# Performance work log

Measured on AMD Instinct MI355X. Metric: run time of the kernel, lower is better.

Reference implementation:

```python
import jax, jax.numpy as jnp
import numpy as np

NUM_HEADS = 8
WINDOW = 7
DILATION = 1
EPS = 1e-5


def channel_ln(x, w, b):
    # x: [B, C, H, W]; normalize over channel dim (axis=1)
    mu = jnp.mean(x, axis=1, keepdims=True)
    var = jnp.var(x, axis=1, keepdims=True)
    xhat = (x - mu) * jax.lax.rsqrt(var + EPS)
    return xhat * w[None, :, None, None] + b[None, :, None, None]


def local_mask(H, W, window, dilation):
    r = (window // 2) * dilation
    ii, jj = jnp.meshgrid(jnp.arange(H), jnp.arange(W), indexing="ij")
    ii = ii.reshape(-1)
    jj = jj.reshape(-1)
    di = jnp.abs(ii[:, None] - ii[None, :])
    dj = jnp.abs(jj[:, None] - jj[None, :])
    m = (di <= r) & (dj <= r)
    if dilation > 1:
        m = m & (di % dilation == 0) & (dj % dilation == 0)
    return m  # [N, N] bool


def local_attention(x, qkv_w, qkv_b, proj_w, proj_b):
    B, C, H, W = x.shape
    N = H * W
    hd = C // NUM_HEADS
    t = x.reshape(B, C, N).transpose(0, 2, 1)            # [B, N, C]
    qkv = t @ qkv_w.T + qkv_b                            # [B, N, 3C]
    qkv = qkv.reshape(B, N, 3, NUM_HEADS, hd)
    q, k, v = (qkv[:, :, i].transpose(0, 2, 1, 3) for i in range(3))  # [B,h,N,d]
    scale = 1.0 / jnp.sqrt(jnp.asarray(hd, x.dtype))
    scores = jnp.einsum("bhnd,bhmd->bhnm", q, k) * scale  # [B,h,N,N]
    mask = local_mask(H, W, WINDOW, DILATION)             # [N,N]
    scores = jnp.where(mask[None, None], scores, jnp.asarray(-jnp.inf, x.dtype))
    attn = jax.nn.softmax(scores, axis=-1)
    out = jnp.einsum("bhnm,bhmd->bhnd", attn, v)          # [B,h,N,d]
    out = out.transpose(0, 2, 1, 3).reshape(B, N, C)      # [B,N,C]
    out = out @ proj_w.T + proj_b
    return out.transpose(0, 2, 1).reshape(B, C, H, W)


def mlp2d(x, fc1_w, fc1_b, fc2_w, fc2_b):
    # 1x1 convs == per-pixel linear over channels
    h = jnp.einsum("bchw,oc->bohw", x, fc1_w) + fc1_b[None, :, None, None]
    h = jax.nn.gelu(h, approximate=False)
    return jnp.einsum("bchw,oc->bohw", h, fc2_w) + fc2_b[None, :, None, None]


def setup_inputs() -> dict:
    key = jax.random.key(0)
    ks = jax.random.split(key, 12)
    B, C, H, W = 1, 256, 56, 56
    hidden = 4 * C
    s = lambda fan: 1.0 / np.sqrt(fan)
    return {
        "x": jax.random.normal(ks[0], (B, C, H, W), jnp.float32),
        "norm1_w": jnp.ones((C,), jnp.float32),
        "norm1_b": jnp.zeros((C,), jnp.float32),
        "qkv_w": jax.random.normal(ks[1], (3 * C, C), jnp.float32) * s(C),
        "qkv_b": jnp.zeros((3 * C,), jnp.float32),
        "proj_w": jax.random.normal(ks[2], (C, C), jnp.float32) * s(C),
        "proj_b": jnp.zeros((C,), jnp.float32),
        "norm2_w": jnp.ones((C,), jnp.float32),
        "norm2_b": jnp.zeros((C,), jnp.float32),
        "fc1_w": jax.random.normal(ks[3], (hidden, C), jnp.float32) * s(C),
        "fc1_b": jnp.zeros((hidden,), jnp.float32),
        "fc2_w": jax.random.normal(ks[4], (C, hidden), jnp.float32) * s(hidden),
        "fc2_b": jnp.zeros((C,), jnp.float32),
    }


def reference(x, norm1_w, norm1_b, qkv_w, qkv_b, proj_w, proj_b,
              norm2_w, norm2_b, fc1_w, fc1_b, fc2_w, fc2_b):
    x = x + local_attention(channel_ln(x, norm1_w, norm1_b), qkv_w, qkv_b, proj_w, proj_b)
    x = x + mlp2d(channel_ln(x, norm2_w, norm2_b), fc1_w, fc1_b, fc2_w, fc2_b)
    return x
```

## Files before the change

### kernel.cpp

```cpp
#include <hip/hip_runtime.h>
#include <math.h>


typedef unsigned int uint;
typedef unsigned short ushort;
typedef unsigned long long u64;
typedef __attribute__((ext_vector_type(8))) short short8;
typedef __attribute__((ext_vector_type(4))) float floatx4;
typedef __attribute__((ext_vector_type(4))) unsigned short ushort4v;

#define AS1(p) (const __attribute__((address_space(1))) void*)(p)
#define AS3(p) (__attribute__((address_space(3))) void*)(p)

__device__ __forceinline__ float bf2f(ushort u) {
  union { uint i; float f; } v; v.i = ((uint)u) << 16; return v.f;
}
__device__ __forceinline__ ushort f2bf(float f) {
  union { float f; uint i; } v; v.f = f;
  uint u = v.i;
  return (ushort)((u + 0x7fffu + ((u >> 16) & 1u)) >> 16);
}

__device__ __forceinline__ void stage64(const ushort* src, int kstride,
                                        ushort* dstBase, int tid) {
  const int srow = tid >> 5;
  const int scb  = (tid & 31) ^ srow;
  const ushort* g = src + (size_t)srow * kstride + scb * 8;
  ushort* d = dstBase + tid * 8;
  #pragma unroll
  for (int r = 0; r < 8; ++r) {
    __builtin_amdgcn_global_load_lds(AS1(g), AS3(d), 16, 0, 0);
    g += 8 * kstride;
    d += 2048;
  }
}

__device__ __forceinline__ void compute64(const ushort* As, const ushort* Bs,
                                          int w, int lane, floatx4 acc[4]) {
  const int fm = lane & 15;
  const int q  = lane >> 4;
  const int swz = fm & 7;
  const int arow = (w * 16 + fm) * 256;
  #pragma unroll
  for (int kt = 0; kt < 8; ++kt) {
    const int blk = ((kt * 4 + q) ^ swz) * 8;
    short8 af = *(const short8*)&As[arow + blk];
    #pragma unroll
    for (int nt = 0; nt < 4; ++nt) {
      short8 bfr = *(const short8*)&Bs[(nt * 16 + fm) * 256 + blk];
      acc[nt] = __builtin_amdgcn_mfma_f32_16x16x32_bf16(af, bfr, acc[nt], 0, 0, 0);
    }
  }
}

__global__ __launch_bounds__(256) void prep_kernel(
    const float* __restrict__ x, const float* __restrict__ n1w,
    const float* __restrict__ n1b,
    const float* __restrict__ qkvw, const float* __restrict__ projw,
    const float* __restrict__ f1w, const float* __restrict__ f2w,
    float* __restrict__ xT, ushort* __restrict__ t1, ushort* __restrict__ wcat)
{
  const int tid = threadIdx.x;
  const int bid = blockIdx.x;
  if (bid >= 196) {
    int idx = (bid - 196) * 256 + tid;
    float v;
    if (idx < 196608)       v = qkvw[idx];
    else if (idx < 262144)  v = projw[idx - 196608];
    else if (idx < 524288)  v = f1w[idx - 262144];
    else                    v = f2w[idx - 524288];
    wcat[idx] = f2bf(v);
    return;
  }
  __shared__ float tile[256 * 17];
  __shared__ float red[2][16][16];
  __shared__ float mu[16], rsv[16];
  const int n0 = bid * 16;
  const int px = tid & 15, grp = tid >> 4;
  #pragma unroll 4
  for (int it = 0; it < 16; ++it) {
    int c = it * 16 + grp;
    tile[c * 17 + px] = x[(size_t)c * 3136 + n0 + px];
  }
  __syncthreads();
  float s = 0.f, ss = 0.f;
  #pragma unroll
  for (int i = 0; i < 16; ++i) {
    float v = tile[(grp * 16 + i) * 17 + px];
    s += v; ss += v * v;
  }
  red[0][px][grp] = s; red[1][px][grp] = ss;
  __syncthreads();
  if (tid < 16) {
    float s2 = 0.f, ss2 = 0.f;
    #pragma unroll
    for (int g = 0; g < 16; ++g) { s2 += red[0][tid][g]; ss2 += red[1][tid][g]; }
    float m = s2 * (1.f / 256.f);
    float var = ss2 * (1.f / 256.f) - m * m;
    mu[tid] = m;
    rsv[tid] = rsqrtf(var + 1e-5f);
  }
  __syncthreads();
  const float wc = n1w[tid], bc = n1b[tid];
  #pragma unroll 4
  for (int p = 0; p < 16; ++p) {
    float v = tile[tid * 17 + p];
    xT[(size_t)(n0 + p) * 256 + tid] = v;
    t1[(size_t)(n0 + p) * 256 + tid] = f2bf((v - mu[p]) * rsv[p] * wc + bc);
  }
}

__global__ __launch_bounds__(256, 2) void qkv_kernel(
    const ushort* __restrict__ A, const ushort* __restrict__ B,
    const float* __restrict__ bias, ushort* __restrict__ out)
{
  __shared__ ushort As[16384], Bs[16384];
  const int tid = threadIdx.x, lane = tid & 63, w = tid >> 6;
  const int m0 = blockIdx.y * 64, n0 = blockIdx.x * 64;
  floatx4 acc[4] = {{0.f,0.f,0.f,0.f},{0.f,0.f,0.f,0.f},
                    {0.f,0.f,0.f,0.f},{0.f,0.f,0.f,0.f}};
  stage64(A + (size_t)m0 * 256, 256, As, tid);
  stage64(B + (size_t)n0 * 256, 256, Bs, tid);
  asm volatile("s_waitcnt vmcnt(0)" ::: "memory");
  __syncthreads();
  compute64(As, Bs, w, lane, acc);
  const int fm = lane & 15, q4 = (lane >> 4) * 4;
  #pragma unroll
  for (int nt = 0; nt < 4; ++nt)
    #pragma unroll
    for (int r = 0; r < 4; ++r) {
      int m = m0 + w * 16 + q4 + r;
      int n = n0 + nt * 16 + fm;
      float v = acc[nt][r] + bias[n];
      if (n < 256) v *= 0.17677669529663687f;
      out[(size_t)m * 768 + n] = f2bf(v);
    }
}

#define ATTN_SMEM 144416

__global__ __launch_bounds__(256, 1) void attnproj_kernel(
    const ushort* __restrict__ qkv, const ushort* __restrict__ pw_bf,
    const float* __restrict__ projb, const float* __restrict__ xT,
    float* __restrict__ x1)
{
  __shared__ __align__(16) char smem[ATTN_SMEM];
  ushort* Kh  = (ushort*)smem;
  ushort* Vh  = (ushort*)(smem + 52000);
  float*  pr  = (float*)(smem + 103200);
  ushort* aas = (ushort*)(smem + 135968);
  ushort* Bs0 = (ushort*)smem;
  ushort* Bs1 = (ushort*)(smem + 103200);

  const int tid = threadIdx.x;
  const int i0 = (blockIdx.x / 14) * 4, j0 = (blockIdx.x % 14) * 4;

  for (int s = tid; s < 3200; s += 256) {
    int p = s >> 5, ck = s & 31;
    int ii = i0 - 3 + p / 10, jj = j0 - 3 + p % 10;
    if (ii >= 0 && ii < 56 && jj >= 0 && jj < 56) {
      const ushort* kr = qkv + (size_t)(ii * 56 + jj) * 768 + 256 + ck * 8;
      short8 kv = *(const short8*)kr;
      u64 lo = ((const u64*)&kv)[0], hi = ((const u64*)&kv)[1];
      *(u64*)&Kh[p * 260 + ck * 8] = lo;
      *(u64*)&Kh[p * 260 + ck * 8 + 4] = hi;
      *(short8*)&Vh[p * 256 + ck * 8] = *(const short8*)(kr + 256);
    } else {
      *(u64*)&Kh[p * 260 + ck * 8] = 0ull;
      *(u64*)&Kh[p * 260 + ck * 8 + 4] = 0ull;
      short8 z = {0, 0, 0, 0, 0, 0, 0, 0};
      *(short8*)&Vh[p * 256 + ck * 8] = z;
    }
  }
  __syncthreads();

  const int wv = tid >> 6, lane = tid & 63;
  const int h = lane >> 3, mg = lane & 7;
  for (int qq = 0; qq < 4; ++qq) {
    const int p = wv * 4 + qq;
    const int qi = p >> 2, qj = p & 3;
    const int iq = i0 + qi, jq = j0 + qj;
    const ushort* qp = qkv + (size_t)(iq * 56 + jq) * 768 + h * 32;
    float qf[32];
    #pragma unroll
    for (int u = 0; u < 4; ++u) {
      short8 qv = *(const short8*)(qp + u * 8);
      #pragma unroll
      for (int e = 0; e < 8; ++e) qf[u * 8 + e] = bf2f((ushort)qv[e]);
    }
    float sv[7];
    float mx = -1e30f;
    #pragma unroll
    for (int k = 0; k < 7; ++k) {
      int m = mg + 8 * k;
      float s = -1e30f;
      if (m < 49) {
        int mi = m / 7, mj = m % 7;
        int ii = iq + mi - 3, jj = jq + mj - 3;
        if (ii >= 0 && ii < 56 && jj >= 0 && jj < 56) {
          int hrow = (qi + mi) * 10 + (qj + mj);
          const u64* k8 = (const u64*)&Kh[hrow * 260 + h * 32];
          float a = 0.f;
          #pragma unroll
          for (int u = 0; u < 8; ++u) {
            u64 kv = k8[u];
            #pragma unroll
            for (int e = 0; e < 4; ++e)
              a += qf[u * 4 + e] * bf2f((ushort)(kv >> (16 * e)));
          }
          s = a;
        }
      }
      sv[k] = s;
      mx = fmaxf(mx, s);
    }
    mx = fmaxf(mx, __shfl_xor(mx, 1));
    mx = fmaxf(mx, __shfl_xor(mx, 2));
    mx = fmaxf(mx, __shfl_xor(mx, 4));
    float sm = 0.f;
    #pragma unroll
    for (int k = 0; k < 7; ++k) { sv[k] = __expf(sv[k] - mx); sm += sv[k]; }
    sm += __shfl_xor(sm, 1);
    sm += __shfl_xor(sm, 2);
    sm += __shfl_xor(sm, 4);
    float inv = 1.f / sm;
    #pragma unroll
    for (int k = 0; k < 7; ++k) {
      int m = mg + 8 * k;
      pr[(p * 8 + h) * 64 + m] = sv[k] * inv;
    }
  }
  __syncthreads();

  stage64(pw_bf, 256, Bs0, tid);

  {
    const int qsel = tid >> 5, cg = tid & 31, hh = cg >> 2;
    #pragma unroll
    for (int pass = 0; pass < 2; ++pass) {
      const int p = pass * 8 + qsel;
      const int qi = p >> 2, qj = p & 3;
      float acc8[8] = {0, 0, 0, 0, 0, 0, 0, 0};
      #pragma unroll
      for (int mi = 0; mi < 7; ++mi)
        #pragma unroll
        for (int mj = 0; mj < 7; ++mj) {
          int m = mi * 7 + mj;
          int hrow = (qi + mi) * 10 + (qj + mj);
          float pm = pr[(p * 8 + hh) * 64 + m];
          short8 v8 = *(const short8*)&Vh[hrow * 256 + cg * 8];
          #pragma unroll
          for (int e = 0; e < 8; ++e)
            acc8[e] += pm * bf2f((ushort)v8[e]);
        }
      short8 o;
      #pragma unroll
      for (int e = 0; e < 8; ++e) o[e] = (short)f2bf(acc8[e]);
      *(short8*)&aas[p * 264 + cg * 8] = o;
    }
  }
  __syncthreads();

  const int fm = lane & 15, q = lane >> 4, q4 = q * 4;
  for (int c = 0; c < 4; ++c) {
    if (c > 0) __syncthreads();
    if (c < 3) {
      stage64(pw_bf + (size_t)(c + 1) * 64 * 256, 256, (c & 1) ? Bs0 : Bs1, tid);
      asm volatile("s_waitcnt vmcnt(8)" ::: "memory");
    } else {
      asm volatile("s_waitcnt vmcnt(0)" ::: "memory");
    }
    __syncthreads();
    const ushort* Bc = (c & 1) ? Bs1 : Bs0;
    floatx4 acc = {0.f, 0.f, 0.f, 0.f};
    const int rr = wv * 16 + fm;
    #pragma unroll
    for (int kt = 0; kt < 8; ++kt) {
      short8 af = *(const short8*)&aas[fm * 264 + kt * 32 + q * 8];
      short8 bfr = *(const short8*)&Bc[rr * 256 + (((kt * 4 + q) ^ (fm & 7))) * 8];
      acc = __builtin_amdgcn_mfma_f32_16x16x32_bf16(af, bfr, acc, 0, 0, 0);
    }
    const int ch = c * 64 + wv * 16 + fm;
    #pragma unroll
    for (int r = 0; r < 4; ++r) {
      int p = q4 + r;
      int n = (i0 + (p >> 2)) * 56 + j0 + (p & 3);
      x1[(size_t)n * 256 + ch] = acc[r] + projb[ch] + xT[(size_t)n * 256 + ch];
    }
  }
}

__global__ __launch_bounds__(256, 2) void fc1_kernel(
    const float* __restrict__ x1, const ushort* __restrict__ B,
    const float* __restrict__ n2w, const float* __restrict__ n2b,
    const float* __restrict__ bias, ushort* __restrict__ out)
{
  __shared__ ushort As[16384], Bs[16384];
  __shared__ float stats[128];
  const int tid = threadIdx.x, lane = tid & 63, w = tid >> 6;
  const int m0 = blockIdx.y * 64, n0 = blockIdx.x * 64;

  stage64(B + (size_t)n0 * 256, 256, Bs, tid);

  {
    const int r = tid >> 2, seg = tid & 3;
    const float* src = x1 + (size_t)(m0 + r) * 256 + seg * 64;
    float s = 0.f, ss = 0.f;
    #pragma unroll
    for (int i = 0; i < 16; ++i) {
      floatx4 v = *(const floatx4*)(src + i * 4);
      s += v[0] + v[1] + v[2] + v[3];
      ss += v[0]*v[0] + v[1]*v[1] + v[2]*v[2] + v[3]*v[3];
    }
    s += __shfl_xor(s, 1); ss += __shfl_xor(ss, 1);
    s += __shfl_xor(s, 2); ss += __shfl_xor(ss, 2);
    if (seg == 0) {
      float mu = s * (1.f / 256.f);
      float var = ss * (1.f / 256.f) - mu * mu;
      stats[r * 2] = mu;
      stats[r * 2 + 1] = rsqrtf(var + 1e-5f);
    }
  }
  __syncthreads();
  #pragma unroll
  for (int k = 0; k < 8; ++k) {
    int s = tid + k * 256;
    int row = s >> 5, cb = s & 31;
    int gb = cb ^ (row & 7);
    float mu = stats[row * 2], rs = stats[row * 2 + 1];
    const float* src = x1 + (size_t)(m0 + row) * 256 + gb * 8;
    floatx4 a = *(const floatx4*)(src);
    floatx4 b2 = *(const floatx4*)(src + 4);
    floatx4 w1 = *(const floatx4*)(n2w + gb * 8);
    floatx4 w2 = *(const floatx4*)(n2w + gb * 8 + 4);
    floatx4 b1v = *(const floatx4*)(n2b + gb * 8);
    floatx4 b2v = *(const floatx4*)(n2b + gb * 8 + 4);
    short8 o;
    #pragma unroll
    for (int e = 0; e < 4; ++e) {
      o[e]     = (short)f2bf((a[e]  - mu) * rs * w1[e] + b1v[e]);
      o[e + 4] = (short)f2bf((b2[e] - mu) * rs * w2[e] + b2v[e]);
    }
    *(short8*)&As[row * 256 + cb * 8] = o;
  }
  asm volatile("s_waitcnt vmcnt(0)" ::: "memory");
  __syncthreads();

  floatx4 acc[4] = {{0.f,0.f,0.f,0.f},{0.f,0.f,0.f,0.f},
                    {0.f,0.f,0.f,0.f},{0.f,0.f,0.f,0.f}};
  compute64(As, Bs, w, lane, acc);
  const int fm = lane & 15, q4 = (lane >> 4) * 4;
  #pragma unroll
  for (int nt = 0; nt < 4; ++nt)
    #pragma unroll
    for (int r = 0; r < 4; ++r) {
      int m = m0 + w * 16 + q4 + r;
      int n = n0 + nt * 16 + fm;
      float v = acc[nt][r] + bias[n];
      v = 0.5f * v * (1.0f + erff(v * 0.70710678118654752f));
      out[(size_t)m * 1024 + n] = f2bf(v);
    }
}

__global__ __launch_bounds__(256, 2) void fc2_kernel(
    const ushort* __restrict__ A, const ushort* __restrict__ B,
    const float* __restrict__ bias, const float* __restrict__ x1,
    float* __restrict__ outf)
{
  __shared__ ushort As[16384], Bs[16384];
  const int tid = threadIdx.x, lane = tid & 63, w = tid >> 6;
  const int m0 = blockIdx.y * 64, n0 = blockIdx.x * 64;
  floatx4 acc[4] = {{0.f,0.f,0.f,0.f},{0.f,0.f,0.f,0.f},
                    {0.f,0.f,0.f,0.f},{0.f,0.f,0.f,0.f}};
  for (int kc = 0; kc < 4; ++kc) {
    if (kc) __syncthreads();
    stage64(A + (size_t)m0 * 1024 + kc * 256, 1024, As, tid);
    stage64(B + (size_t)n0 * 1024 + kc * 256, 1024, Bs, tid);
    asm volatile("s_waitcnt vmcnt(0)" ::: "memory");
    __syncthreads();
    compute64(As, Bs, w, lane, acc);
  }
  const int fm = lane & 15, q4 = (lane >> 4) * 4;
  #pragma unroll
  for (int nt = 0; nt < 4; ++nt)
    #pragma unroll
    for (int r = 0; r < 4; ++r) {
      int m = m0 + w * 16 + q4 + r;
      int n = n0 + nt * 16 + fm;
      outf[(size_t)m * 3136 + n] = acc[nt][r] + bias[m] + x1[(size_t)n * 256 + m];
    }
}

extern "C" void kernel_launch(void* const* d_in, const int* in_sizes, int n_in,
                              void* d_out, int out_size, void* d_ws, size_t ws_size,
                              hipStream_t stream) {
  const float* x     = (const float*)d_in[0];
  const float* n1w   = (const float*)d_in[1];
  const float* n1b   = (const float*)d_in[2];
  const float* qkvw  = (const float*)d_in[3];
  const float* qkvb  = (const float*)d_in[4];
  const float* projw = (const float*)d_in[5];
  const float* projb = (const float*)d_in[6];
  const float* n2w   = (const float*)d_in[7];
  const float* n2b   = (const float*)d_in[8];
  const float* f1w   = (const float*)d_in[9];
  const float* f1b   = (const float*)d_in[10];
  const float* f2w   = (const float*)d_in[11];
  const float* f2b   = (const float*)d_in[12];

  char* ws = (char*)d_ws;
  ushort* wcat = (ushort*)(ws + 0);
  float*  xT   = (float*)(ws + 1572864);
  ushort* t    = (ushort*)(ws + 4784128);
  ushort* qh   = (ushort*)(ws + 6389760);
  float*  x1   = (float*)(ws + 12812288);

  const ushort* qw_bf = wcat;
  const ushort* pw_bf = wcat + 196608;
  const ushort* f1_bf = wcat + 262144;
  const ushort* f2_bf = wcat + 524288;
  float* outf = (float*)d_out;

  hipLaunchKernelGGL(prep_kernel, dim3(3268), dim3(256), 0, stream,
                     x, n1w, n1b, qkvw, projw, f1w, f2w, xT, t, wcat);
  hipLaunchKernelGGL(qkv_kernel, dim3(12, 49), dim3(256), 0, stream,
                     t, qw_bf, qkvb, qh);
  hipLaunchKernelGGL(attnproj_kernel, dim3(196), dim3(256), 0, stream,
                     qh, pw_bf, projb, xT, x1);
  hipLaunchKernelGGL(fc1_kernel, dim3(16, 49), dim3(256), 0, stream,
                     x1, f1_bf, n2w, n2b, f1b, qh);
  hipLaunchKernelGGL(fc2_kernel, dim3(49, 4), dim3(256), 0, stream,
                     f2_bf, qh, f2b, x1, outf);
}
```

Baseline: 147.5 us.

## Fuse LN2, fc1, GELU and fc2 into one per-16-pixel MLP kernel

Replaces the separate fc1 and fc2 kernels with a single mlp_kernel in which each block handles 16 pixels. The block computes the channel LayerNorm, runs fc1 with GELU into a 16x1024 bf16 hidden buffer in LDS, then runs fc2 and adds the bias and residual. This removes the global round trip of the hidden activation and one launch. Weights are streamed through per-wave double-buffered LDS slabs with global_load_lds. In exchange every block re-reads the full fc1 and fc2 weights, the M tile is small (16), and only 196 blocks are launched, which lowers MFMA reuse and occupancy.

```diff
diff --git a/kernel.cpp b/kernel.cpp
--- a/kernel.cpp
+++ b/kernel.cpp
@@ -290,105 +290,165 @@
   }
 }
 
-__global__ __launch_bounds__(256, 2) void fc1_kernel(
-    const float* __restrict__ x1, const ushort* __restrict__ B,
-    const float* __restrict__ n2w, const float* __restrict__ n2b,
-    const float* __restrict__ bias, ushort* __restrict__ out)
+__global__ __launch_bounds__(256, 2) void mlp_kernel(
+    const float* __restrict__ x1, const ushort* __restrict__ f1_bf,
+    const float* __restrict__ f1b, const ushort* __restrict__ f2_bf,
+    const float* __restrict__ f2b, const float* __restrict__ n2w,
+    const float* __restrict__ n2b, float* __restrict__ outf)
 {
-  __shared__ ushort As[16384], Bs[16384];
-  __shared__ float stats[128];
-  const int tid = threadIdx.x, lane = tid & 63, w = tid >> 6;
-  const int m0 = blockIdx.y * 64, n0 = blockIdx.x * 64;
-
-  stage64(B + (size_t)n0 * 256, 256, Bs, tid);
-
+  __shared__ ushort t2s[16 * 256];
+  __shared__ ushort hbuf[16 * 1024];
+  __shared__ ushort slab[4][2][2048];
+  __shared__ float pstat[4][16][2];
+  __shared__ float stats[16][2];
+
+  const int tid = threadIdx.x;
+  const int n0 = blockIdx.x * 16;
+  const int w = tid >> 6;
+  const int lane = tid & 63;
+  const int fm = lane & 15;
+  const int px = tid & 15;
+  const int q = (lane >> 4) & 3;
+  const int l4 = lane >> 2, lb = lane & 3;
+
+  floatx4 xv[4];
+  #pragma unroll
+  for (int mc = 0; mc < 4; ++mc)
+    xv[mc] = *(const floatx4*)(x1 + (size_t)(n0 + px) * 256 + w * 64 + mc * 16 + q * 4);
+  float s = 0.f, ss = 0.f;
+  #pragma unroll
+  for (int mc = 0; mc < 4; ++mc)
+    #pragma unroll
+    for (int e = 0; e < 4; ++e) { s += xv[mc][e]; ss += xv[mc][e] * xv[mc][e]; }
+  s += __shfl_xor(s, 16); ss += __shfl_xor(ss, 16);
+  s += __shfl_xor(s, 32); ss += __shfl_xor(ss, 32);
+  if (lane < 16) { pstat[w][px][0] = s; pstat[w][px][1] = ss; }
+  __syncthreads();
+  if (tid < 16) {
+    float s2 = 0.f, ss2 = 0.f;
+    #pragma unroll
+    for (int ww = 0; ww < 4; ++ww) { s2 += pstat[ww][tid][0]; ss2 += pstat[ww][tid][1]; }
+    float mu = s2 * (1.f / 256.f);
+    float var = ss2 * (1.f / 256.f) - mu * mu;
+    stats[tid][0] = mu;
+    stats[tid][1] = rsqrtf(var + 1e-5f);
+  }
+  __syncthreads();
   {
-    const int r = tid >> 2, seg = tid & 3;
-    const float* src = x1 + (size_t)(m0 + r) * 256 + seg * 64;
-    float s = 0.f, ss = 0.f;
-    #pragma unroll
-    for (int i = 0; i < 16; ++i) {
-      floatx4 v = *(const floatx4*)(src + i * 4);
-      s += v[0] + v[1] + v[2] + v[3];
-      ss += v[0]*v[0] + v[1]*v[1] + v[2]*v[2] + v[3]*v[3];
-    }
-    s += __shfl_xor(s, 1); ss += __shfl_xor(ss, 1);
-    s += __shfl_xor(s, 2); ss += __shfl_xor(ss, 2);
-    if (seg == 0) {
-      float mu = s * (1.f / 256.f);
-      float var = ss * (1.f / 256.f) - mu * mu;
-      stats[r * 2] = mu;
-      stats[r * 2 + 1] = rsqrtf(var + 1e-5f);
-    }
-  }
-  __syncthreads();
-  #pragma unroll
-  for (int k = 0; k < 8; ++k) {
-    int s = tid + k * 256;
-    int row = s >> 5, cb = s & 31;
-    int gb = cb ^ (row & 7);
-    float mu = stats[row * 2], rs = stats[row * 2 + 1];
-    const float* src = x1 + (size_t)(m0 + row) * 256 + gb * 8;
-    floatx4 a = *(const floatx4*)(src);
-    floatx4 b2 = *(const floatx4*)(src + 4);
-    floatx4 w1 = *(const floatx4*)(n2w + gb * 8);
-    floatx4 w2 = *(const floatx4*)(n2w + gb * 8 + 4);
-    floatx4 b1v = *(const floatx4*)(n2b + gb * 8);
-    floatx4 b2v = *(const floatx4*)(n2b + gb * 8 + 4);
-    short8 o;
-    #pragma unroll
-    for (int e = 0; e < 4; ++e) {
-      o[e]     = (short)f2bf((a[e]  - mu) * rs * w1[e] + b1v[e]);
-      o[e + 4] = (short)f2bf((b2[e] - mu) * rs * w2[e] + b2v[e]);
-    }
-    *(short8*)&As[row * 256 + cb * 8] = o;
-  }
-  asm volatile("s_waitcnt vmcnt(0)" ::: "memory");
-  __syncthreads();
-
-  floatx4 acc[4] = {{0.f,0.f,0.f,0.f},{0.f,0.f,0.f,0.f},
-                    {0.f,0.f,0.f,0.f},{0.f,0.f,0.f,0.f}};
-  compute64(As, Bs, w, lane, acc);
-  const int fm = lane & 15, q4 = (lane >> 4) * 4;
-  #pragma unroll
-  for (int nt = 0; nt < 4; ++nt)
-    #pragma unroll
-    for (int r = 0; r < 4; ++r) {
-      int m = m0 + w * 16 + q4 + r;
-      int n = n0 + nt * 16 + fm;
-      float v = acc[nt][r] + bias[n];
-      v = 0.5f * v * (1.0f + erff(v * 0.70710678118654752f));
-      out[(size_t)m * 1024 + n] = f2bf(v);
-    }
-}
-
-__global__ __launch_bounds__(256, 2) void fc2_kernel(
-    const ushort* __restrict__ A, const ushort* __restrict__ B,
-    const float* __restrict__ bias, const float* __restrict__ x1,
-    float* __restrict__ outf)
-{
-  __shared__ ushort As[16384], Bs[16384];
-  const int tid = threadIdx.x, lane = tid & 63, w = tid >> 6;
-  const int m0 = blockIdx.y * 64, n0 = blockIdx.x * 64;
-  floatx4 acc[4] = {{0.f,0.f,0.f,0.f},{0.f,0.f,0.f,0.f},
-                    {0.f,0.f,0.f,0.f},{0.f,0.f,0.f,0.f}};
-  for (int kc = 0; kc < 4; ++kc) {
-    if (kc) __syncthreads();
-    stage64(A + (size_t)m0 * 1024 + kc * 256, 1024, As, tid);
-    stage64(B + (size_t)n0 * 1024 + kc * 256, 1024, Bs, tid);
-    asm volatile("s_waitcnt vmcnt(0)" ::: "memory");
-    __syncthreads();
-    compute64(As, Bs, w, lane, acc);
-  }
-  const int fm = lane & 15, q4 = (lane >> 4) * 4;
-  #pragma unroll
-  for (int nt = 0; nt < 4; ++nt)
-    #pragma unroll
-    for (int r = 0; r < 4; ++r) {
-      int m = m0 + w * 16 + q4 + r;
-      int n = n0 + nt * 16 + fm;
-      outf[(size_t)m * 3136 + n] = acc[nt][r] + bias[m] + x1[(size_t)n * 256 + m];
-    }
+    float mu = stats[px][0], rs = stats[px][1];
+    #pragma unroll
+    for (int mc = 0; mc < 4; ++mc) {
+      int ch0 = w * 64 + mc * 16 + q * 4;
+      ushort4v o;
+      #pragma unroll
+      for (int e = 0; e < 4; ++e)
+        o[e] = f2bf((xv[mc][e] - mu) * rs * n2w[ch0 + e] + n2b[ch0 + e]);
+      int slot = (ch0 >> 3) ^ (px & 7);
+      *(ushort4v*)&t2s[px * 256 + slot * 8 + (ch0 & 7)] = o;
+    }
+  }
+  float f1br[4][4];
+  #pragma unroll
+  for (int ci = 0; ci < 4; ++ci)
+    #pragma unroll
+    for (int nt = 0; nt < 4; ++nt)
+      f1br[ci][nt] = f1b[(ci * 4 + w) * 64 + nt * 16 + fm];
+  __syncthreads();
+
+  ushort* sb0 = slab[w][0];
+  ushort* sb1 = slab[w][1];
+
+  {
+    #define STAGE_F1(nc, kt, buf) do { \
+      _Pragma("unroll") \
+      for (int i_ = 0; i_ < 4; ++i_) { \
+        int row_ = i_ * 16 + l4; \
+        const ushort* g_ = f1_bf + (size_t)((nc) * 64 + row_) * 256 + (kt) * 32 + (lb ^ (row_ & 3)) * 8; \
+        __builtin_amdgcn_global_load_lds(AS1(g_), AS3((buf) + i_ * 512 + lane * 8), 16, 0, 0); \
+      } } while (0)
+
+    floatx4 fa[4] = {{0.f,0.f,0.f,0.f},{0.f,0.f,0.f,0.f},
+                     {0.f,0.f,0.f,0.f},{0.f,0.f,0.f,0.f}};
+    STAGE_F1(w, 0, sb0);
+    for (int sidx = 0; sidx < 32; ++sidx) {
+      const int kt = sidx & 7;
+      const int nc = (sidx >> 3) * 4 + w;
+      ushort* cur = (sidx & 1) ? sb1 : sb0;
+      ushort* nxt = (sidx & 1) ? sb0 : sb1;
+      if (sidx < 31) {
+        int s1 = sidx + 1;
+        STAGE_F1((s1 >> 3) * 4 + w, s1 & 7, nxt);
+        asm volatile("s_waitcnt vmcnt(4)" ::: "memory");
+      } else {
+        asm volatile("s_waitcnt vmcnt(0)" ::: "memory");
+      }
+      short8 af = *(const short8*)&t2s[fm * 256 + (((kt * 4 + q) ^ (fm & 7)) * 8)];
+      #pragma unroll
+      for (int nt = 0; nt < 4; ++nt) {
+        int r = nt * 16 + fm;
+        short8 bfr = *(const short8*)&cur[r * 32 + (q ^ (r & 3)) * 8];
+        fa[nt] = __builtin_amdgcn_mfma_f32_16x16x32_bf16(af, bfr, fa[nt], 0, 0, 0);
+      }
+      if (kt == 7) {
+        #pragma unroll
+        for (int nt = 0; nt < 4; ++nt) {
+          int hc = nc * 64 + nt * 16 + fm;
+          int hslotbase = (hc >> 3);
+          #pragma unroll
+          for (int r4 = 0; r4 < 4; ++r4) {
+            int prow = q * 4 + r4;
+            float v = fa[nt][r4] + f1br[sidx >> 3][nt];
+            v = 0.5f * v * (1.0f + erff(v * 0.70710678118654752f));
+            hbuf[prow * 1024 + ((hslotbase ^ (prow & 7)) * 8) + (hc & 7)] = f2bf(v);
+            fa[nt][r4] = 0.f;
+          }
+        }
+      }
+    }
+    #undef STAGE_F1
+  }
+  __syncthreads();
+
+  {
+    #define STAGE_F2(kt, buf) do { \
+      _Pragma("unroll") \
+      for (int i_ = 0; i_ < 4; ++i_) { \
+        int row_ = i_ * 16 + l4; \
+        const ushort* g_ = f2_bf + (size_t)(w * 64 + row_) * 1024 + (kt) * 32 + (lb ^ (row_ & 3)) * 8; \
+        __builtin_amdgcn_global_load_lds(AS1(g_), AS3((buf) + i_ * 512 + lane * 8), 16, 0, 0); \
+      } } while (0)
+
+    floatx4 ga[4] = {{0.f,0.f,0.f,0.f},{0.f,0.f,0.f,0.f},
+                     {0.f,0.f,0.f,0.f},{0.f,0.f,0.f,0.f}};
+    STAGE_F2(0, sb0);
+    for (int kt = 0; kt < 32; ++kt) {
+      ushort* cur = (kt & 1) ? sb1 : sb0;
+      ushort* nxt = (kt & 1) ? sb0 : sb1;
+      if (kt < 31) {
+        STAGE_F2(kt + 1, nxt);
+        asm volatile("s_waitcnt vmcnt(4)" ::: "memory");
+      } else {
+        asm volatile("s_waitcnt vmcnt(0)" ::: "memory");
+      }
+      short8 bfr = *(const short8*)&hbuf[fm * 1024 + (((kt * 4 + q) ^ (fm & 7)) * 8)];
+      #pragma unroll
+      for (int mt = 0; mt < 4; ++mt) {
+        int r = mt * 16 + fm;
+        short8 af = *(const short8*)&cur[r * 32 + (q ^ (r & 3)) * 8];
+        ga[mt] = __builtin_amdgcn_mfma_f32_16x16x32_bf16(af, bfr, ga[mt], 0, 0, 0);
+      }
+    }
+    #undef STAGE_F2
+    #pragma unroll
+    for (int mt = 0; mt < 4; ++mt) {
+      #pragma unroll
+      for (int r4 = 0; r4 < 4; ++r4) {
+        int ch = w * 64 + mt * 16 + q * 4 + r4;
+        float v = ga[mt][r4] + f2b[ch] + xv[mt][r4];
+        outf[(size_t)ch * 3136 + n0 + fm] = v;
+      }
+    }
+  }
 }
 
 extern "C" void kernel_launch(void* const* d_in, const int* in_sizes, int n_in,
@@ -427,8 +487,6 @@
                      t, qw_bf, qkvb, qh);
   hipLaunchKernelGGL(attnproj_kernel, dim3(196), dim3(256), 0, stream,
                      qh, pw_bf, projb, xT, x1);
-  hipLaunchKernelGGL(fc1_kernel, dim3(16, 49), dim3(256), 0, stream,
-                     x1, f1_bf, n2w, n2b, f1b, qh);
-  hipLaunchKernelGGL(fc2_kernel, dim3(49, 4), dim3(256), 0, stream,
-                     f2_bf, qh, f2b, x1, outf);
-}
+  hipLaunchKernelGGL(mlp_kernel, dim3(196), dim3(256), 0, stream,
+                     x1, f1_bf, f1b, f2_bf, f2b, n2w, n2b, outf);
+}
```

Result: no change. 145.1 us (-1.6%).
